# Optimization experiments

Hardware: AMD Instinct MI355X
Metric: run time of the kernel (lower is better)

## Reference

```python
import jax, jax.numpy as jnp
import numpy as np

D_MODEL = 1024
N_HEADS = 16
D_HEAD = 64
NUM_REL_POS = 2047
B = 8
L = 1024


def setup_inputs() -> dict:
    key = jax.random.key(0)
    ks = jax.random.split(key, 8)
    s = 1.0 / np.sqrt(D_MODEL)
    x = jax.random.normal(ks[0], (B, L, D_MODEL), dtype=jnp.float32)
    rel_indices = jax.random.randint(ks[1], (L, L), 0, NUM_REL_POS)
    Wq = jax.random.normal(ks[2], (D_MODEL, D_MODEL), dtype=jnp.float32) * s
    Wk = jax.random.normal(ks[3], (D_MODEL, D_MODEL), dtype=jnp.float32) * s
    Wv = jax.random.normal(ks[4], (D_MODEL, D_MODEL), dtype=jnp.float32) * s
    Wo = jax.random.normal(ks[5], (D_MODEL, D_MODEL), dtype=jnp.float32) * s
    rel_k = jax.random.normal(ks[6], (NUM_REL_POS, D_HEAD), dtype=jnp.float32) * 0.02
    rel_v = jax.random.normal(ks[7], (NUM_REL_POS, D_HEAD), dtype=jnp.float32) * 0.02
    return {"x": x, "rel_indices": rel_indices, "Wq": Wq, "Wk": Wk,
            "Wv": Wv, "Wo": Wo, "rel_k": rel_k, "rel_v": rel_v}


def reference(x, rel_indices, Wq, Wk, Wv, Wo, rel_k, rel_v):
    Bz, Ls, D = x.shape
    H, dk = N_HEADS, D_HEAD
    scale = 1.0 / np.sqrt(dk)
    # torch Linear: y = x @ W.T, weights are [out, in]
    q = jnp.einsum('bld,ed->ble', x, Wq).reshape(Bz, Ls, H, dk).transpose(0, 2, 1, 3)
    k = jnp.einsum('bld,ed->ble', x, Wk).reshape(Bz, Ls, H, dk).transpose(0, 2, 1, 3)
    v = jnp.einsum('bld,ed->ble', x, Wv).reshape(Bz, Ls, H, dk).transpose(0, 2, 1, 3)
    r_k = rel_k[rel_indices]  # (L, L, dk)
    r_v = rel_v[rel_indices]  # (L, L, dk)
    content = jnp.einsum('bhid,bhjd->bhij', q, k)
    rel = jnp.einsum('bhid,ijd->bhij', q, r_k)
    scores = (content + rel) * scale
    probs = jax.nn.softmax(scores, axis=-1)  # dropout = 0 (eval)
    out = jnp.einsum('bhij,bhjd->bhid', probs, v) + jnp.einsum('bhij,ijd->bhid', probs, r_v)
    out = out.transpose(0, 2, 1, 3).reshape(Bz, Ls, D)
    return jnp.einsum('bld,ed->ble', out, Wo)
```

## Files before the change

### kernel.cpp

```cpp
#include <hip/hip_runtime.h>

#define B_ 8
#define H_ 16
#define L_ 1024
#define DH_ 64
#define DM_ 1024
#define NP_ 2047
#define NP2_ 2048
#define SCALE_ 0.125f

#define PS_ 1032
#define HS_ 260

typedef __attribute__((ext_vector_type(8))) short bf16x8;
typedef __attribute__((ext_vector_type(4))) float f32x4;

__device__ __forceinline__ unsigned short f2bf(float x) {
    union { float f; unsigned int u; } v; v.f = x;
    return (unsigned short)((v.u + 0x7FFFu + ((v.u >> 16) & 1u)) >> 16);
}
__device__ __forceinline__ float bf2f(unsigned short b) {
    union { unsigned int u; float f; } v; v.u = ((unsigned int)b) << 16;
    return v.f;
}

template <int MODE>
__global__ __launch_bounds__(256) void proj_gemm(const float* __restrict__ X,
                                                 const float* __restrict__ W,
                                                 float* __restrict__ Yf,
                                                 unsigned short* __restrict__ Y0,
                                                 unsigned short* __restrict__ Y1)
{
    __shared__ __align__(16) float As[16][68];
    __shared__ __align__(16) float Bs[16][68];
    const int t   = threadIdx.x;
    const int tm  = t & 15;
    const int tn  = t >> 4;
    const int row0 = blockIdx.x * 64;
    const int col0 = blockIdx.y * 64;
    const int lr = t >> 2;
    const int lc = (t & 3) * 4;

    float acc[4][4];
#pragma unroll
    for (int i = 0; i < 4; ++i)
#pragma unroll
        for (int j = 0; j < 4; ++j) acc[i][j] = 0.f;

    for (int k0 = 0; k0 < DM_; k0 += 16) {
        float4 av = *(const float4*)(X + (size_t)(row0 + lr) * DM_ + k0 + lc);
        float4 wv = *(const float4*)(W + (size_t)(col0 + lr) * DM_ + k0 + lc);
        __syncthreads();
        As[lc + 0][lr] = av.x; As[lc + 1][lr] = av.y;
        As[lc + 2][lr] = av.z; As[lc + 3][lr] = av.w;
        Bs[lc + 0][lr] = wv.x; Bs[lc + 1][lr] = wv.y;
        Bs[lc + 2][lr] = wv.z; Bs[lc + 3][lr] = wv.w;
        __syncthreads();
#pragma unroll
        for (int kk = 0; kk < 16; ++kk) {
            float4 a  = *(const float4*)&As[kk][tm * 4];
            float4 w4 = *(const float4*)&Bs[kk][tn * 4];
            acc[0][0] = fmaf(a.x, w4.x, acc[0][0]);
            acc[0][1] = fmaf(a.x, w4.y, acc[0][1]);
            acc[0][2] = fmaf(a.x, w4.z, acc[0][2]);
            acc[0][3] = fmaf(a.x, w4.w, acc[0][3]);
            acc[1][0] = fmaf(a.y, w4.x, acc[1][0]);
            acc[1][1] = fmaf(a.y, w4.y, acc[1][1]);
            acc[1][2] = fmaf(a.y, w4.z, acc[1][2]);
            acc[1][3] = fmaf(a.y, w4.w, acc[1][3]);
            acc[2][0] = fmaf(a.z, w4.x, acc[2][0]);
            acc[2][1] = fmaf(a.z, w4.y, acc[2][1]);
            acc[2][2] = fmaf(a.z, w4.z, acc[2][2]);
            acc[2][3] = fmaf(a.z, w4.w, acc[2][3]);
            acc[3][0] = fmaf(a.w, w4.x, acc[3][0]);
            acc[3][1] = fmaf(a.w, w4.y, acc[3][1]);
            acc[3][2] = fmaf(a.w, w4.z, acc[3][2]);
            acc[3][3] = fmaf(a.w, w4.w, acc[3][3]);
        }
    }

    const int h = blockIdx.y;
#pragma unroll
    for (int i = 0; i < 4; ++i) {
        const int row = row0 + tm * 4 + i;
        if (MODE == 1) {
            float4 r = make_float4(acc[i][0], acc[i][1], acc[i][2], acc[i][3]);
            *(float4*)(Yf + (size_t)row * DM_ + col0 + tn * 4) = r;
        } else {
            const int bb = row >> 10;
            const int l  = row & 1023;
            if (MODE == 0) {
                ushort4 hi4, lo4;
                unsigned short* hp = (unsigned short*)&hi4;
                unsigned short* lp = (unsigned short*)&lo4;
#pragma unroll
                for (int j = 0; j < 4; ++j) {
                    unsigned short hb = f2bf(acc[i][j]);
                    hp[j] = hb;
                    lp[j] = f2bf(acc[i][j] - bf2f(hb));
                }
                const size_t base = (((size_t)bb * H_ + h) * L_ + l) * DH_ + tn * 4;
                *(ushort4*)(Y0 + base) = hi4;
                *(ushort4*)(Y1 + base) = lo4;
            } else {
#pragma unroll
                for (int j = 0; j < 4; ++j) {
                    const int d = tn * 4 + j;
                    Y0[(((size_t)bb * H_ + h) * DH_ + d) * L_ + l] = f2bf(acc[i][j]);
                }
            }
        }
    }
}

__global__ __launch_bounds__(256) void prep_rel(const float* __restrict__ rk,
                                                const float* __restrict__ rv,
                                                unsigned short* __restrict__ rk_hi,
                                                unsigned short* __restrict__ rv_t)
{
    const int idx = blockIdx.x * 256 + threadIdx.x;
    const int p = idx >> 6;
    const int d = idx & 63;
    float xk = (p < NP_) ? rk[(size_t)p * DH_ + d] : 0.f;
    rk_hi[idx] = f2bf(xk);
    float xv = (p < NP_) ? rv[(size_t)p * DH_ + d] : 0.f;
    rv_t[(size_t)d * NP2_ + p] = f2bf(xv);
}

__global__ __launch_bounds__(512, 4) void shaw_attn_mfma(
    const unsigned short* __restrict__ qh, const unsigned short* __restrict__ ql,
    const unsigned short* __restrict__ kh, const unsigned short* __restrict__ kl,
    const unsigned short* __restrict__ vt, const int* __restrict__ ridx,
    const unsigned short* __restrict__ rkh, const unsigned short* __restrict__ rvt,
    float* __restrict__ out)
{
    __shared__ __align__(16) unsigned char regionA[16 * PS_ * 2];
    __shared__ __align__(16) unsigned char regionB[16 * HS_ * 4];
    __shared__ float pmax[16][8];
    __shared__ float psum[16][8];

    char*           qrel8 = (char*)regionA;
    unsigned short* Pu    = (unsigned short*)regionA;
    float*          hist  = (float*)regionB;
    float*          red   = (float*)regionB;

    const int t    = threadIdx.x;
    const int w    = t >> 6;
    const int lane = t & 63;
    const int mrow = lane & 15;
    const int grp  = lane >> 4;
    const int i0   = blockIdx.x * 16;
    const int h    = blockIdx.y;
    const int b    = blockIdx.z;
    const size_t bh = (size_t)b * H_ + h;

    const unsigned short* qhp = qh + bh * (size_t)(L_ * DH_);
    const unsigned short* qlp = ql + bh * (size_t)(L_ * DH_);
    const unsigned short* khp = kh + bh * (size_t)(L_ * DH_);
    const unsigned short* klp = kl + bh * (size_t)(L_ * DH_);
    const unsigned short* vtp = vt + bh * (size_t)(DH_ * L_);

    bf16x8 qAh[2], qAl[2];
#pragma unroll
    for (int s = 0; s < 2; ++s) {
        const size_t off = (size_t)(i0 + mrow) * DH_ + s * 32 + grp * 8;
        qAh[s] = *(const bf16x8*)(qhp + off);
        qAl[s] = *(const bf16x8*)(qlp + off);
    }

    {
        const unsigned short* rb = rkh + (size_t)(w * 256 + mrow) * DH_ + grp * 8;
#pragma unroll 4
        for (int tt = 0; tt < 16; ++tt) {
            bf16x8 Bh0 = *(const bf16x8*)(rb + tt * 1024);
            bf16x8 Bh1 = *(const bf16x8*)(rb + tt * 1024 + 32);
            f32x4 c = {0.f, 0.f, 0.f, 0.f};
            c = __builtin_amdgcn_mfma_f32_16x16x32_bf16(qAh[0], Bh0, c, 0, 0, 0);
            c = __builtin_amdgcn_mfma_f32_16x16x32_bf16(qAh[1], Bh1, c, 0, 0, 0);
            const int pcol = (w * 16 + tt) * 16 + mrow;
            unsigned int pk = 0;
#pragma unroll
            for (int r = 0; r < 4; ++r) {
                int qi = (int)rintf(c[r] * 128.f);
                qi = qi > 127 ? 127 : (qi < -127 ? -127 : qi);
                pk |= ((unsigned int)(qi & 0xff)) << (8 * r);
            }
            *(unsigned int*)(qrel8 + pcol * 16 + grp * 4) = pk;
        }
    }
    __syncthreads();

    float sc[8][4];
    {
        const unsigned short* kbh = khp + (size_t)(w * 128 + mrow) * DH_ + grp * 8;
        const unsigned short* kbl = klp + (size_t)(w * 128 + mrow) * DH_ + grp * 8;
#pragma unroll 2
        for (int tt = 0; tt < 8; ++tt) {
            bf16x8 Bh0 = *(const bf16x8*)(kbh + tt * 1024);
            bf16x8 Bh1 = *(const bf16x8*)(kbh + tt * 1024 + 32);
            bf16x8 Bl0 = *(const bf16x8*)(kbl + tt * 1024);
            bf16x8 Bl1 = *(const bf16x8*)(kbl + tt * 1024 + 32);
            f32x4 c = {0.f, 0.f, 0.f, 0.f};
            c = __builtin_amdgcn_mfma_f32_16x16x32_bf16(qAh[0], Bh0, c, 0, 0, 0);
            c = __builtin_amdgcn_mfma_f32_16x16x32_bf16(qAh[1], Bh1, c, 0, 0, 0);
            c = __builtin_amdgcn_mfma_f32_16x16x32_bf16(qAh[0], Bl0, c, 0, 0, 0);
            c = __builtin_amdgcn_mfma_f32_16x16x32_bf16(qAh[1], Bl1, c, 0, 0, 0);
            c = __builtin_amdgcn_mfma_f32_16x16x32_bf16(qAl[0], Bh0, c, 0, 0, 0);
            c = __builtin_amdgcn_mfma_f32_16x16x32_bf16(qAl[1], Bh1, c, 0, 0, 0);
#pragma unroll
            for (int r = 0; r < 4; ++r) sc[tt][r] = c[r] * SCALE_;
        }
    }

#pragma unroll
    for (int tt = 0; tt < 8; ++tt) {
        const int jcol = (w * 8 + tt) * 16 + mrow;
#pragma unroll
        for (int r = 0; r < 4; ++r) {
            const int pidx = ridx[(size_t)(i0 + grp * 4 + r) * L_ + jcol];
            sc[tt][r] = fmaf((float)qrel8[pidx * 16 + grp * 4 + r], SCALE_ / 128.f, sc[tt][r]);
        }
    }

    float mx[4];
#pragma unroll
    for (int r = 0; r < 4; ++r) {
        float m = sc[0][r];
#pragma unroll
        for (int tt = 1; tt < 8; ++tt) m = fmaxf(m, sc[tt][r]);
#pragma unroll
        for (int off = 1; off < 16; off <<= 1) m = fmaxf(m, __shfl_xor(m, off));
        mx[r] = m;
    }
    {
        const float wv0 = (mrow == 0) ? mx[0] : (mrow == 1) ? mx[1] : (mrow == 2) ? mx[2] : mx[3];
        if (mrow < 4) pmax[grp * 4 + mrow][w] = wv0;
    }
    __syncthreads();

    float gm[4];
#pragma unroll
    for (int r = 0; r < 4; ++r) {
        const int rr = grp * 4 + r;
        float m = pmax[rr][0];
#pragma unroll
        for (int u = 1; u < 8; ++u) m = fmaxf(m, pmax[rr][u]);
        gm[r] = m;
    }
    float sm[4] = {0.f, 0.f, 0.f, 0.f};
#pragma unroll
    for (int tt = 0; tt < 8; ++tt) {
        const int jcol = (w * 8 + tt) * 16 + mrow;
#pragma unroll
        for (int r = 0; r < 4; ++r) {
            const float e = __expf(sc[tt][r] - gm[r]);
            sm[r] += e;
            Pu[(grp * 4 + r) * PS_ + jcol] = f2bf(e);
        }
    }
#pragma unroll
    for (int r = 0; r < 4; ++r) {
#pragma unroll
        for (int off = 1; off < 16; off <<= 1) sm[r] += __shfl_xor(sm[r], off);
    }
    {
        const float sv0 = (mrow == 0) ? sm[0] : (mrow == 1) ? sm[1] : (mrow == 2) ? sm[2] : sm[3];
        if (mrow < 4) psum[grp * 4 + mrow][w] = sv0;
    }
    __syncthreads();

    const int n = w & 3;
    const int khalf = w >> 2;
    f32x4 acc = {0.f, 0.f, 0.f, 0.f};
    {
        const unsigned short* vcol = vtp + (size_t)(n * 16 + mrow) * L_ + khalf * 512 + grp * 8;
#pragma unroll 4
        for (int s = 0; s < 16; ++s) {
            bf16x8 a  = *(const bf16x8*)(Pu + mrow * PS_ + khalf * 512 + s * 32 + grp * 8);
            bf16x8 bb = *(const bf16x8*)(vcol + s * 32);
            acc = __builtin_amdgcn_mfma_f32_16x16x32_bf16(a, bb, acc, 0, 0, 0);
        }
    }

    for (int pass = 0; pass < 8; ++pass) {
        {
            float4* h4 = (float4*)hist;
            const float4 z4 = make_float4(0.f, 0.f, 0.f, 0.f);
            for (int z = t; z < (16 * HS_) / 4; z += 512) h4[z] = z4;
        }
        __syncthreads();
#pragma unroll
        for (int tt = 0; tt < 8; ++tt) {
            const int jcol = (w * 8 + tt) * 16 + mrow;
#pragma unroll
            for (int r = 0; r < 4; ++r) {
                const int rr = grp * 4 + r;
                const int pidx = ridx[(size_t)(i0 + rr) * L_ + jcol];
                if ((pidx >> 8) == pass)
                    atomicAdd(&hist[rr * HS_ + (pidx & 255)], bf2f(Pu[rr * PS_ + jcol]));
            }
        }
        __syncthreads();
        const unsigned short* rvcol =
            rvt + (size_t)(n * 16 + mrow) * NP2_ + pass * 256 + khalf * 128 + grp * 8;
#pragma unroll
        for (int s = 0; s < 4; ++s) {
            const int kb = khalf * 128 + s * 32;
            const f32x4* hp = (const f32x4*)&hist[mrow * HS_ + kb + grp * 8];
            f32x4 h0 = hp[0], h1 = hp[1];
            bf16x8 a;
#pragma unroll
            for (int e = 0; e < 4; ++e) { a[e] = (short)f2bf(h0[e]); a[e + 4] = (short)f2bf(h1[e]); }
            bf16x8 bb = *(const bf16x8*)(rvcol + s * 32);
            acc = __builtin_amdgcn_mfma_f32_16x16x32_bf16(a, bb, acc, 0, 0, 0);
        }
        __syncthreads();
    }

#pragma unroll
    for (int r = 0; r < 4; ++r) red[w * 320 + (grp * 4 + r) * 20 + mrow] = acc[r];
    __syncthreads();
    if (w < 4) {
#pragma unroll
        for (int r = 0; r < 4; ++r) {
            const int rr = grp * 4 + r;
            float o = red[w * 320 + rr * 20 + mrow] + red[(w + 4) * 320 + rr * 20 + mrow];
            float ssum = 0.f;
#pragma unroll
            for (int u = 0; u < 8; ++u) ssum += psum[rr][u];
            out[((size_t)b * L_ + i0 + rr) * DM_ + h * DH_ + w * 16 + mrow] = o / ssum;
        }
    }
}

extern "C" void kernel_launch(void* const* d_in, const int* in_sizes, int n_in,
                              void* d_out, int out_size, void* d_ws, size_t ws_size,
                              hipStream_t stream)
{
    const float* x    = (const float*)d_in[0];
    const int*   ridx = (const int*)  d_in[1];
    const float* Wq   = (const float*)d_in[2];
    const float* Wk   = (const float*)d_in[3];
    const float* Wv   = (const float*)d_in[4];
    const float* Wo   = (const float*)d_in[5];
    const float* rk   = (const float*)d_in[6];
    const float* rv   = (const float*)d_in[7];
    float* out = (float*)d_out;

    const size_t NQ = (size_t)B_ * H_ * L_ * DH_;
    float* attn = (float*)d_ws;
    unsigned short* u = (unsigned short*)(attn + NQ);
    unsigned short* qh = u;            u += NQ;
    unsigned short* ql = u;            u += NQ;
    unsigned short* kh = u;            u += NQ;
    unsigned short* kl = u;            u += NQ;
    unsigned short* vt = u;            u += NQ;
    unsigned short* rkh = u;           u += (size_t)NP2_ * DH_;
    unsigned short* rvt = u;           u += (size_t)NP2_ * DH_;

    dim3 gthr(256);
    dim3 ggrid((B_ * L_) / 64, DM_ / 64);

    prep_rel<<<dim3((NP2_ * DH_) / 256), gthr, 0, stream>>>(rk, rv, rkh, rvt);
    proj_gemm<0><<<ggrid, gthr, 0, stream>>>(x, Wq, nullptr, qh, ql);
    proj_gemm<0><<<ggrid, gthr, 0, stream>>>(x, Wk, nullptr, kh, kl);
    proj_gemm<2><<<ggrid, gthr, 0, stream>>>(x, Wv, nullptr, vt, nullptr);

    shaw_attn_mfma<<<dim3(L_ / 16, H_, B_), dim3(512), 0, stream>>>(
        qh, ql, kh, kl, vt, ridx, rkh, rvt, attn);

    proj_gemm<1><<<ggrid, gthr, 0, stream>>>(attn, Wo, out, nullptr, nullptr);
}
```

Baseline: 2.265 ms.

## Enlarge projection GEMM tiles to 128x128 with 8x8 per-thread outputs and register prefetch

The fp32 projection GEMM moves from 64x64 block tiles with 4x4 per-thread accumulators to 128x128 tiles with 8x8 accumulators. The next k-slice is prefetched into registers while the current one is computed. The V-transpose epilogue now writes vectorized ushort4 along L instead of scalar stores. The aim is more arithmetic per shared-memory and global load in the four projection GEMMs, at the cost of higher register pressure and a quarter as many blocks.

Result: faster. 2.148 ms (-5.2%).

```diff
diff --git a/kernel.cpp b/kernel.cpp
--- a/kernel.cpp
+++ b/kernel.cpp
@@ -31,83 +31,103 @@
                                                  unsigned short* __restrict__ Y0,
                                                  unsigned short* __restrict__ Y1)
 {
-    __shared__ __align__(16) float As[16][68];
-    __shared__ __align__(16) float Bs[16][68];
+    __shared__ __align__(16) float As[16][132];
+    __shared__ __align__(16) float Bs[16][132];
     const int t   = threadIdx.x;
     const int tm  = t & 15;
     const int tn  = t >> 4;
-    const int row0 = blockIdx.x * 64;
-    const int col0 = blockIdx.y * 64;
-    const int lr = t >> 2;
-    const int lc = (t & 3) * 4;
-
-    float acc[4][4];
-#pragma unroll
-    for (int i = 0; i < 4; ++i)
-#pragma unroll
-        for (int j = 0; j < 4; ++j) acc[i][j] = 0.f;
+    const int row0 = blockIdx.x * 128;
+    const int col0 = blockIdx.y * 128;
+    const int lr  = t >> 1;
+    const int lc  = (t & 1) * 8;
+
+    float acc[8][8];
+#pragma unroll
+    for (int i = 0; i < 8; ++i)
+#pragma unroll
+        for (int j = 0; j < 8; ++j) acc[i][j] = 0.f;
+
+    float4 xa, xb, wa, wb;
+    const float* xp = X + (size_t)(row0 + lr) * DM_ + lc;
+    const float* wp = W + (size_t)(col0 + lr) * DM_ + lc;
+    xa = *(const float4*)(xp);     xb = *(const float4*)(xp + 4);
+    wa = *(const float4*)(wp);     wb = *(const float4*)(wp + 4);
 
     for (int k0 = 0; k0 < DM_; k0 += 16) {
-        float4 av = *(const float4*)(X + (size_t)(row0 + lr) * DM_ + k0 + lc);
-        float4 wv = *(const float4*)(W + (size_t)(col0 + lr) * DM_ + k0 + lc);
-        __syncthreads();
-        As[lc + 0][lr] = av.x; As[lc + 1][lr] = av.y;
-        As[lc + 2][lr] = av.z; As[lc + 3][lr] = av.w;
-        Bs[lc + 0][lr] = wv.x; Bs[lc + 1][lr] = wv.y;
-        Bs[lc + 2][lr] = wv.z; Bs[lc + 3][lr] = wv.w;
-        __syncthreads();
+        __syncthreads();
+        As[lc + 0][lr] = xa.x; As[lc + 1][lr] = xa.y; As[lc + 2][lr] = xa.z; As[lc + 3][lr] = xa.w;
+        As[lc + 4][lr] = xb.x; As[lc + 5][lr] = xb.y; As[lc + 6][lr] = xb.z; As[lc + 7][lr] = xb.w;
+        Bs[lc + 0][lr] = wa.x; Bs[lc + 1][lr] = wa.y; Bs[lc + 2][lr] = wa.z; Bs[lc + 3][lr] = wa.w;
+        Bs[lc + 4][lr] = wb.x; Bs[lc + 5][lr] = wb.y; Bs[lc + 6][lr] = wb.z; Bs[lc + 7][lr] = wb.w;
+        __syncthreads();
+        if (k0 + 16 < DM_) {
+            xa = *(const float4*)(xp + k0 + 16);  xb = *(const float4*)(xp + k0 + 20);
+            wa = *(const float4*)(wp + k0 + 16);  wb = *(const float4*)(wp + k0 + 20);
+        }
 #pragma unroll
         for (int kk = 0; kk < 16; ++kk) {
-            float4 a  = *(const float4*)&As[kk][tm * 4];
-            float4 w4 = *(const float4*)&Bs[kk][tn * 4];
-            acc[0][0] = fmaf(a.x, w4.x, acc[0][0]);
-            acc[0][1] = fmaf(a.x, w4.y, acc[0][1]);
-            acc[0][2] = fmaf(a.x, w4.z, acc[0][2]);
-            acc[0][3] = fmaf(a.x, w4.w, acc[0][3]);
-            acc[1][0] = fmaf(a.y, w4.x, acc[1][0]);
-            acc[1][1] = fmaf(a.y, w4.y, acc[1][1]);
-            acc[1][2] = fmaf(a.y, w4.z, acc[1][2]);
-            acc[1][3] = fmaf(a.y, w4.w, acc[1][3]);
-            acc[2][0] = fmaf(a.z, w4.x, acc[2][0]);
-            acc[2][1] = fmaf(a.z, w4.y, acc[2][1]);
-            acc[2][2] = fmaf(a.z, w4.z, acc[2][2]);
-            acc[2][3] = fmaf(a.z, w4.w, acc[2][3]);
-            acc[3][0] = fmaf(a.w, w4.x, acc[3][0]);
-            acc[3][1] = fmaf(a.w, w4.y, acc[3][1]);
-            acc[3][2] = fmaf(a.w, w4.z, acc[3][2]);
-            acc[3][3] = fmaf(a.w, w4.w, acc[3][3]);
-        }
-    }
-
-    const int h = blockIdx.y;
-#pragma unroll
-    for (int i = 0; i < 4; ++i) {
-        const int row = row0 + tm * 4 + i;
-        if (MODE == 1) {
-            float4 r = make_float4(acc[i][0], acc[i][1], acc[i][2], acc[i][3]);
-            *(float4*)(Yf + (size_t)row * DM_ + col0 + tn * 4) = r;
-        } else {
-            const int bb = row >> 10;
-            const int l  = row & 1023;
-            if (MODE == 0) {
+            float4 a0 = *(const float4*)&As[kk][tm * 4];
+            float4 a1 = *(const float4*)&As[kk][64 + tm * 4];
+            float4 b0 = *(const float4*)&Bs[kk][tn * 8];
+            float4 b1 = *(const float4*)&Bs[kk][tn * 8 + 4];
+            const float av[8] = {a0.x, a0.y, a0.z, a0.w, a1.x, a1.y, a1.z, a1.w};
+            const float bv[8] = {b0.x, b0.y, b0.z, b0.w, b1.x, b1.y, b1.z, b1.w};
+#pragma unroll
+            for (int i = 0; i < 8; ++i)
+#pragma unroll
+                for (int j = 0; j < 8; ++j)
+                    acc[i][j] = fmaf(av[i], bv[j], acc[i][j]);
+        }
+    }
+
+    const int bidx = row0 >> 10;
+    const int hbase = blockIdx.y * 2 + (tn >> 3);
+    const int dbase = (tn & 7) * 8;
+
+    if constexpr (MODE == 1) {
+#pragma unroll
+        for (int i = 0; i < 8; ++i) {
+            const int row = row0 + ((i < 4) ? (tm * 4 + i) : (64 + tm * 4 + i - 4));
+            *(float4*)(Yf + (size_t)row * DM_ + col0 + tn * 8)     = make_float4(acc[i][0], acc[i][1], acc[i][2], acc[i][3]);
+            *(float4*)(Yf + (size_t)row * DM_ + col0 + tn * 8 + 4) = make_float4(acc[i][4], acc[i][5], acc[i][6], acc[i][7]);
+        }
+    }
+    if constexpr (MODE == 0) {
+#pragma unroll
+        for (int i = 0; i < 8; ++i) {
+            const int row = row0 + ((i < 4) ? (tm * 4 + i) : (64 + tm * 4 + i - 4));
+            const int l = row & 1023;
+            const size_t base = (((size_t)bidx * H_ + hbase) * L_ + l) * DH_ + dbase;
+#pragma unroll
+            for (int jh = 0; jh < 2; ++jh) {
                 ushort4 hi4, lo4;
                 unsigned short* hp = (unsigned short*)&hi4;
                 unsigned short* lp = (unsigned short*)&lo4;
 #pragma unroll
                 for (int j = 0; j < 4; ++j) {
-                    unsigned short hb = f2bf(acc[i][j]);
+                    const float y = acc[i][jh * 4 + j];
+                    unsigned short hb = f2bf(y);
                     hp[j] = hb;
-                    lp[j] = f2bf(acc[i][j] - bf2f(hb));
+                    lp[j] = f2bf(y - bf2f(hb));
                 }
-                const size_t base = (((size_t)bb * H_ + h) * L_ + l) * DH_ + tn * 4;
-                *(ushort4*)(Y0 + base) = hi4;
-                *(ushort4*)(Y1 + base) = lo4;
-            } else {
-#pragma unroll
-                for (int j = 0; j < 4; ++j) {
-                    const int d = tn * 4 + j;
-                    Y0[(((size_t)bb * H_ + h) * DH_ + d) * L_ + l] = f2bf(acc[i][j]);
-                }
+                *(ushort4*)(Y0 + base + jh * 4) = hi4;
+                *(ushort4*)(Y1 + base + jh * 4) = lo4;
+            }
+        }
+    }
+    if constexpr (MODE == 2) {
+#pragma unroll
+        for (int j = 0; j < 8; ++j) {
+            const int d = dbase + j;
+            const size_t cb = ((size_t)(bidx * H_ + hbase) * DH_ + d) * L_;
+#pragma unroll
+            for (int half = 0; half < 2; ++half) {
+                const int l0 = (row0 & 1023) + half * 64 + tm * 4;
+                ushort4 v4;
+                unsigned short* vp = (unsigned short*)&v4;
+#pragma unroll
+                for (int i = 0; i < 4; ++i) vp[i] = f2bf(acc[half * 4 + i][j]);
+                *(ushort4*)(Y0 + cb + l0) = v4;
             }
         }
     }
@@ -359,7 +379,7 @@
     unsigned short* rvt = u;           u += (size_t)NP2_ * DH_;
 
     dim3 gthr(256);
-    dim3 ggrid((B_ * L_) / 64, DM_ / 64);
+    dim3 ggrid((B_ * L_) / 128, DM_ / 128);
 
     prep_rel<<<dim3((NP2_ * DH_) / 256), gthr, 0, stream>>>(rk, rv, rkh, rvt);
     proj_gemm<0><<<ggrid, gthr, 0, stream>>>(x, Wq, nullptr, qh, ql);
```
